# Kernel tuning notes

Measured on AMD Instinct MI355X. Metric: run time of the kernel, lower is better.

## Reference

```python
import jax, jax.numpy as jnp
import numpy as np

N = 50000
E = 800000
F_IN = 256
C = 64  # embedding_size, heads=1
EDGE_DIM = 2
NEG_SLOPE = 0.01


def setup_inputs() -> dict:
    key = jax.random.key(0)
    ks = jax.random.split(key, 12)
    s = 1.0 / np.sqrt(C)
    return {
        "x": jax.random.normal(ks[0], (N, F_IN), jnp.float32),
        "edge_index": jax.random.randint(ks[1], (2, E), 0, N, jnp.int64),
        "edge_attr": jax.random.normal(ks[2], (E, EDGE_DIM), jnp.float32),
        "Wf": jax.random.normal(ks[3], (F_IN, C), jnp.float32) / np.sqrt(F_IN),
        "bf": jnp.zeros((C,), jnp.float32),
        "Wq": jax.random.normal(ks[4], (C, C), jnp.float32) * s,
        "bq": jnp.zeros((C,), jnp.float32),
        "Wk": jax.random.normal(ks[5], (C, C), jnp.float32) * s,
        "bk": jnp.zeros((C,), jnp.float32),
        "Wv": jax.random.normal(ks[6], (C, C), jnp.float32) * s,
        "bv": jnp.zeros((C,), jnp.float32),
        "We": jax.random.normal(ks[7], (EDGE_DIM, C), jnp.float32) / np.sqrt(EDGE_DIM),
        "Wskip": jax.random.normal(ks[8], (C, C), jnp.float32) * s,
        "bskip": jnp.zeros((C,), jnp.float32),
    }


def reference(x, edge_index, edge_attr, Wf, bf, Wq, bq, Wk, bk, Wv, bv, We, Wskip, bskip):
    n = x.shape[0]
    src, dst = edge_index[0], edge_index[1]
    inv_sqrt_c = 1.0 / np.sqrt(C)

    h = jax.nn.leaky_relu(x @ Wf + bf, NEG_SLOPE)
    e = edge_attr @ We  # [E, C] edge embedding (lin_edge, no bias), same each layer

    for _ in range(3):
        q = h @ Wq + bq
        k = h @ Wk + bk
        v = h @ Wv + bv
        kj = k[src] + e                                  # [E, C] key + edge feat
        alpha = jnp.sum(q[dst] * kj, axis=-1) * inv_sqrt_c  # [E]
        # per-destination softmax
        m = jax.ops.segment_max(alpha, dst, num_segments=n)
        ex = jnp.exp(alpha - m[dst])
        den = jax.ops.segment_sum(ex, dst, num_segments=n)
        a = ex / den[dst]                                # [E]
        msg = (v[src] + e) * a[:, None]                  # [E, C]
        agg = jax.ops.segment_sum(msg, dst, num_segments=n)  # [N, C]
        h = jax.nn.leaky_relu(agg + h @ Wskip + bskip, NEG_SLOPE)  # root_weight skip
    return h
```

## Files before the change

kernel.cpp:

```cpp
#include <hip/hip_runtime.h>
#include <hip/hip_fp16.h>

#define NN 50000
#define NE 800000
#define FIN 256
#define C 64
#define NEG_SLOPE 0.01f
#define SCAN_BLOCKS ((NN + 255) / 256)
#define NBUCK 196
#define BCAP 8192
#define EB_CHUNK 2048
#define EB_BLOCKS ((NE + EB_CHUNK - 1) / EB_CHUNK)

typedef float f32x16 __attribute__((ext_vector_type(16)));

__device__ __forceinline__ float leaky(float v) { return v > 0.f ? v : NEG_SLOPE * v; }

__global__ __launch_bounds__(256) void k_tw(const float* __restrict__ Wq,
                                            const float* __restrict__ Wk,
                                            const float* __restrict__ Wv,
                                            const float* __restrict__ Ws,
                                            float* __restrict__ Wt) {
    const int idx = blockIdx.x * 256 + threadIdx.x;
    if (idx >= 4 * 64 * 64) return;
    const int m = idx >> 12, r = idx & 4095, c = r >> 6, k = r & 63;
    const float* W = (m == 0) ? Wq : (m == 1) ? Wk : (m == 2) ? Wv : Ws;
    Wt[idx] = W[k * 64 + c];
}

__global__ __launch_bounds__(256) void k_feat(const float* __restrict__ x,
                                              const float* __restrict__ Wf,
                                              const float* __restrict__ bf,
                                              float* __restrict__ h) {
    __shared__ float4 Sx[64][33];
    const int t = threadIdx.x;
    const int lane = t & 63;
    const int q = __builtin_amdgcn_readfirstlane(t) >> 6;
    const int base = blockIdx.x * 64;

    const float4* x4 = (const float4*)x;
    float4 acc[4];
#pragma unroll
    for (int cp = 0; cp < 4; ++cp) acc[cp] = make_float4(0.f, 0.f, 0.f, 0.f);

#define FRAG(wreg, xs)                                                      \
    acc[0].x = fmaf(xs, wreg[0],  acc[0].x);                                \
    acc[0].y = fmaf(xs, wreg[1],  acc[0].y);                                \
    acc[0].z = fmaf(xs, wreg[2],  acc[0].z);                                \
    acc[0].w = fmaf(xs, wreg[3],  acc[0].w);                                \
    acc[1].x = fmaf(xs, wreg[4],  acc[1].x);                                \
    acc[1].y = fmaf(xs, wreg[5],  acc[1].y);                                \
    acc[1].z = fmaf(xs, wreg[6],  acc[1].z);                                \
    acc[1].w = fmaf(xs, wreg[7],  acc[1].w);                                \
    acc[2].x = fmaf(xs, wreg[8],  acc[2].x);                                \
    acc[2].y = fmaf(xs, wreg[9],  acc[2].y);                                \
    acc[2].z = fmaf(xs, wreg[10], acc[2].z);                                \
    acc[2].w = fmaf(xs, wreg[11], acc[2].w);                                \
    acc[3].x = fmaf(xs, wreg[12], acc[3].x);                                \
    acc[3].y = fmaf(xs, wreg[13], acc[3].y);                                \
    acc[3].z = fmaf(xs, wreg[14], acc[3].z);                                \
    acc[3].w = fmaf(xs, wreg[15], acc[3].w);

    for (int ph = 0; ph < 2; ++ph) {
#pragma unroll
        for (int i = 0; i < 8; ++i) {
            const int idx = t + i * 256;
            const int row = idx >> 5, c = idx & 31;
            int nn = base + row; if (nn >= NN) nn = NN - 1;
            Sx[row][c] = x4[(size_t)nn * 64 + ph * 32 + c];
        }
        __syncthreads();

        const float* wbase = Wf + (size_t)(ph * 128) * 64 + q * 16;
#pragma unroll
        for (int j = 0; j < 32; ++j) {
            const float4 xv = Sx[lane][j];
            const float* wrow = wbase + (size_t)j * 256;
            f32x16 w0_, w1_, w2_, w3_;
            asm volatile("s_load_dwordx16 %0, %4, 0x0\n\t"
                         "s_load_dwordx16 %1, %4, 0x100\n\t"
                         "s_load_dwordx16 %2, %4, 0x200\n\t"
                         "s_load_dwordx16 %3, %4, 0x300\n\t"
                         "s_waitcnt lgkmcnt(0)"
                         : "=&s"(w0_), "=&s"(w1_), "=&s"(w2_), "=&s"(w3_)
                         : "s"(wrow));
            FRAG(w0_, xv.x)
            FRAG(w1_, xv.y)
            FRAG(w2_, xv.z)
            FRAG(w3_, xv.w)
        }
        __syncthreads();
    }
#undef FRAG

    float4* O = (float4*)Sx;
    const float4* bf4 = (const float4*)bf;
#pragma unroll
    for (int cp = 0; cp < 4; ++cp) {
        const float4 b = bf4[q * 4 + cp];
        float4 r;
        r.x = leaky(acc[cp].x + b.x); r.y = leaky(acc[cp].y + b.y);
        r.z = leaky(acc[cp].z + b.z); r.w = leaky(acc[cp].w + b.w);
        O[lane * 17 + q * 4 + cp] = r;
    }
    __syncthreads();
#pragma unroll
    for (int i = 0; i < 4; ++i) {
        const int idx = t + i * 256;
        const int row = idx >> 4, c = idx & 15;
        const int nn = base + row;
        if (nn < NN) ((float4*)h)[(size_t)nn * 16 + c] = O[row * 17 + c];
    }
}

#define QKVS_NPB 32

__global__ __launch_bounds__(256) void k_qkvs(const float* __restrict__ h,
                                              const float* __restrict__ Wt,
                                              const float* __restrict__ bq,
                                              const float* __restrict__ bk,
                                              const float* __restrict__ bv,
                                              const float* __restrict__ bs,
                                              float* __restrict__ qkvs) {
    __shared__ float4 Sh[QKVS_NPB][16];
    const int t = threadIdx.x;
    const int lane = t & 63;
    const int wid = __builtin_amdgcn_readfirstlane(t) >> 6;
    const int base = blockIdx.x * QKVS_NPB;

    const float4* h4 = (const float4*)h;
#pragma unroll
    for (int i = 0; i < 2; ++i) {
        const int idx = t + i * 256;
        const int row = idx >> 4, c = idx & 15;
        int n = base + row; if (n >= NN) n = NN - 1;
        Sh[row][c] = h4[(size_t)n * 16 + c];
    }

    const bool kv = (wid < 2);
    const int wn = (wid & 1) << 4;

    const int mA = kv ? 1 : 0;
    const int mB = kv ? 2 : 3;
    const float4* wa4 = (const float4*)(Wt + ((size_t)mA << 12) + ((size_t)lane << 6));
    const float4* wb4 = (const float4*)(Wt + ((size_t)mB << 12) + ((size_t)lane << 6));
    float4 wa[16], wb[16];
#pragma unroll
    for (int j = 0; j < 16; ++j) { wa[j] = wa4[j]; wb[j] = wb4[j]; }
    const float biasA = kv ? bk[lane] : bq[lane];
    const float biasB = kv ? bv[lane] : bs[lane];

    __syncthreads();

#pragma unroll 2
    for (int i = 0; i < 16; ++i) {
        const int n = base + wn + i;
        float a0 = 0.f, a1 = 0.f, a2 = 0.f, a3 = 0.f;
        float b0 = 0.f, b1 = 0.f, b2 = 0.f, b3 = 0.f;
#pragma unroll
        for (int j = 0; j < 16; ++j) {
            const float4 xv = Sh[wn + i][j];
            a0 = fmaf(xv.x, wa[j].x, a0); a1 = fmaf(xv.y, wa[j].y, a1);
            a2 = fmaf(xv.z, wa[j].z, a2); a3 = fmaf(xv.w, wa[j].w, a3);
            b0 = fmaf(xv.x, wb[j].x, b0); b1 = fmaf(xv.y, wb[j].y, b1);
            b2 = fmaf(xv.z, wb[j].z, b2); b3 = fmaf(xv.w, wb[j].w, b3);
        }
        const float A = ((a0 + a1) + (a2 + a3)) + biasA;
        const float B = ((b0 + b1) + (b2 + b3)) + biasB;
        if (n < NN) {
            float* orow = qkvs + (size_t)n * 192;
            if (kv) {
                ((__half2*)(orow + 64))[lane] = __floats2half2_rn(A, B);
            } else {
                orow[lane] = A;
                orow[128 + lane] = B;
            }
        }
    }
}

__global__ __launch_bounds__(256) void k_bucket(const int* __restrict__ ei,
                                                const float* __restrict__ eattr,
                                                int* __restrict__ gcur,
                                                uint2* __restrict__ ebuck) {
    __shared__ int hist[NBUCK], lbase[NBUCK], lcur[NBUCK];
    const int t = threadIdx.x;
    const int base = blockIdx.x * EB_CHUNK;
    if (t < NBUCK) { hist[t] = 0; lcur[t] = 0; }
    __syncthreads();

    int dcache[8];
#pragma unroll
    for (int i = 0; i < 8; ++i) {
        const int e = base + i * 256 + t;
        int d = -1;
        if (e < NE) {
            d = ei[NE + e];
            atomicAdd(&hist[d >> 8], 1);
        }
        dcache[i] = d;
    }
    __syncthreads();
    if (t < NBUCK && hist[t] > 0)
        lbase[t] = atomicAdd(&gcur[t], hist[t]);
    __syncthreads();

#pragma unroll
    for (int i = 0; i < 8; ++i) {
        const int e = base + i * 256 + t;
        const int d = dcache[i];
        if (d >= 0) {
            const int b = d >> 8;
            const int rank = atomicAdd(&lcur[b], 1);
            const __half2 a = __floats2half2_rn(eattr[e * 2], eattr[e * 2 + 1]);
            const unsigned src = (unsigned)ei[e];
            ebuck[(size_t)b * BCAP + lbase[b] + rank] =
                make_uint2(((unsigned)d << 16) | src, *(const unsigned*)&a);
        }
    }
}

__global__ __launch_bounds__(256) void k_fin_deg(const int* __restrict__ gcur,
                                                 const uint2* __restrict__ ebuck,
                                                 int* __restrict__ deg) {
    __shared__ int dcnt[256];
    const int t = threadIdx.x;
    const int b = blockIdx.x;
    dcnt[t] = 0;
    __syncthreads();
    const int n = gcur[b];
    for (int i = t; i < n; i += 256) {
        const unsigned x = ebuck[(size_t)b * BCAP + i].x;
        atomicAdd(&dcnt[(x >> 16) & 255], 1);
    }
    __syncthreads();
    const int idx = b * 256 + t;
    if (idx < NN) deg[idx] = dcnt[t];
}

__global__ __launch_bounds__(256) void k_blocksum(const int* __restrict__ deg,
                                                  int* __restrict__ bsum) {
    __shared__ int sh[256];
    const int t = threadIdx.x;
    const int idx = blockIdx.x * 256 + t;
    sh[t] = (idx < NN) ? deg[idx] : 0;
    __syncthreads();
#pragma unroll
    for (int off = 128; off > 0; off >>= 1) {
        if (t < off) sh[t] += sh[t + off];
        __syncthreads();
    }
    if (t == 0) bsum[blockIdx.x] = sh[0];
}

__global__ __launch_bounds__(256) void k_scanb(const int* __restrict__ bsum,
                                               int* __restrict__ boff) {
    __shared__ int sh[256];
    const int t = threadIdx.x;
    const int v = (t < SCAN_BLOCKS) ? bsum[t] : 0;
    sh[t] = v;
    __syncthreads();
#pragma unroll
    for (int off = 1; off < 256; off <<= 1) {
        const int x = (t >= off) ? sh[t - off] : 0;
        __syncthreads();
        sh[t] += x;
        __syncthreads();
    }
    if (t < SCAN_BLOCKS) boff[t] = sh[t] - v;
}

__global__ __launch_bounds__(256) void k_writeptr(const int* __restrict__ deg,
                                                  const int* __restrict__ boff,
                                                  int* __restrict__ row_ptr) {
    __shared__ int sh[256];
    const int t = threadIdx.x;
    const int idx = blockIdx.x * 256 + t;
    const int v = (idx < NN) ? deg[idx] : 0;
    sh[t] = v;
    __syncthreads();
#pragma unroll
    for (int off = 1; off < 256; off <<= 1) {
        const int x = (t >= off) ? sh[t - off] : 0;
        __syncthreads();
        sh[t] += x;
        __syncthreads();
    }
    if (idx < NN) row_ptr[idx] = boff[blockIdx.x] + sh[t] - v;
    if (idx == 0) row_ptr[NN] = NE;
}

__global__ __launch_bounds__(256) void k_fin_scat(const int* __restrict__ gcur,
                                                  const uint2* __restrict__ ebuck,
                                                  const int* __restrict__ row_ptr,
                                                  uint2* __restrict__ erec) {
    __shared__ int pcur[256];
    const int t = threadIdx.x;
    const int b = blockIdx.x;
    const int idx = b * 256 + t;
    pcur[t] = (idx < NN) ? row_ptr[idx] : 0;
    __syncthreads();
    const int n = gcur[b];
    for (int i = t; i < n; i += 256) {
        const uint2 rec = ebuck[(size_t)b * BCAP + i];
        const int d = (rec.x >> 16) & 255;
        const int pos = atomicAdd(&pcur[d], 1);
        erec[pos] = make_uint2(rec.x & 0xFFFFu, rec.y);
    }
}

__global__ __launch_bounds__(256) void k_conv(const int* __restrict__ row_ptr,
                                              const uint2* __restrict__ erec,
                                              const float* __restrict__ We,
                                              const float* __restrict__ qkvs,
                                              float* __restrict__ hout) {
    const int t = threadIdx.x;
    const int lane = t & 63;
    const int g = lane >> 4;
    const int p = lane & 15;
    const int wv = __builtin_amdgcn_readfirstlane(t) >> 6;
    const int d = blockIdx.x * 4 + wv;
    if (d >= NN) return;

    const float* qrow = qkvs + (size_t)d * 192;
    const float4 q4  = *(const float4*)(qrow + 4 * p);
    const float4 w0  = *(const float4*)(We + 4 * p);
    const float4 w1  = *(const float4*)(We + 64 + 4 * p);

    float pg0 = q4.x * w0.x + q4.y * w0.y + q4.z * w0.z + q4.w * w0.w;
    float pg1 = q4.x * w1.x + q4.y * w1.y + q4.z * w1.z + q4.w * w1.w;
#pragma unroll
    for (int mask = 1; mask <= 8; mask <<= 1) {
        pg0 += __shfl_xor(pg0, mask);
        pg1 += __shfl_xor(pg1, mask);
    }
    const float g0 = pg0, g1 = pg1;

    const int i0 = row_ptr[d], i1 = row_ptr[d + 1];
    const char* kvbase = (const char*)qkvs + 256 + ((size_t)p << 4);

    float m = -1e30f, l = 0.f, S1 = 0.f, S2 = 0.f;
    float4 acc = make_float4(0.f, 0.f, 0.f, 0.f);

    int i = i0 + g;
    for (; i + 4 < i1; i += 8) {
        const uint2 ra = erec[i];
        const uint2 rb = erec[i + 4];
        const __half2 aha = *(const __half2*)&ra.y;
        const __half2 ahb = *(const __half2*)&rb.y;
        const float a0a = __low2float(aha), a1a = __high2float(aha);
        const float a0b = __low2float(ahb), a1b = __high2float(ahb);
        const float4 kva = *(const float4*)(kvbase + (size_t)ra.x * 768);
        const float4 kvb = *(const float4*)(kvbase + (size_t)rb.x * 768);
        const __half2* ha = (const __half2*)&kva;
        const __half2* hb = (const __half2*)&kvb;
        const float ka0 = __low2float(ha[0]), va0 = __high2float(ha[0]);
        const float ka1 = __low2float(ha[1]), va1 = __high2float(ha[1]);
        const float ka2 = __low2float(ha[2]), va2 = __high2float(ha[2]);
        const float ka3 = __low2float(ha[3]), va3 = __high2float(ha[3]);
        const float kb0 = __low2float(hb[0]), vb0 = __high2float(hb[0]);
        const float kb1 = __low2float(hb[1]), vb1 = __high2float(hb[1]);
        const float kb2 = __low2float(hb[2]), vb2 = __high2float(hb[2]);
        const float kb3 = __low2float(hb[3]), vb3 = __high2float(hb[3]);
        float da = q4.x * ka0 + q4.y * ka1 + q4.z * ka2 + q4.w * ka3;
        float db = q4.x * kb0 + q4.y * kb1 + q4.z * kb2 + q4.w * kb3;
        da += __shfl_xor(da, 1);  db += __shfl_xor(db, 1);
        da += __shfl_xor(da, 2);  db += __shfl_xor(db, 2);
        da += __shfl_xor(da, 4);  db += __shfl_xor(db, 4);
        da += __shfl_xor(da, 8);  db += __shfl_xor(db, 8);
        const float Pa = (da + g0 * a0a + g1 * a1a) * 0.125f;
        const float Pb = (db + g0 * a0b + g1 * a1b) * 0.125f;
        const float mn = fmaxf(m, fmaxf(Pa, Pb));
        const float s  = __expf(m - mn);
        const float ea = __expf(Pa - mn);
        const float eb = __expf(Pb - mn);
        l = l * s + ea + eb;
        acc.x = acc.x * s + va0 * ea + vb0 * eb;
        acc.y = acc.y * s + va1 * ea + vb1 * eb;
        acc.z = acc.z * s + va2 * ea + vb2 * eb;
        acc.w = acc.w * s + va3 * ea + vb3 * eb;
        S1 = S1 * s + a0a * ea + a0b * eb;
        S2 = S2 * s + a1a * ea + a1b * eb;
        m = mn;
    }
    for (; i < i1; i += 4) {
        const uint2 r = erec[i];
        const __half2 ah = *(const __half2*)&r.y;
        const float a0 = __low2float(ah), a1 = __high2float(ah);
        const float4 kvl = *(const float4*)(kvbase + (size_t)r.x * 768);
        const __half2* hv = (const __half2*)&kvl;
        const float kf0 = __low2float(hv[0]), vf0 = __high2float(hv[0]);
        const float kf1 = __low2float(hv[1]), vf1 = __high2float(hv[1]);
        const float kf2 = __low2float(hv[2]), vf2 = __high2float(hv[2]);
        const float kf3 = __low2float(hv[3]), vf3 = __high2float(hv[3]);
        float dot = q4.x * kf0 + q4.y * kf1 + q4.z * kf2 + q4.w * kf3;
        dot += __shfl_xor(dot, 1);
        dot += __shfl_xor(dot, 2);
        dot += __shfl_xor(dot, 4);
        dot += __shfl_xor(dot, 8);
        const float P = (dot + g0 * a0 + g1 * a1) * 0.125f;
        const float mn = fmaxf(m, P);
        const float s = __expf(m - mn);
        const float e = __expf(P - mn);
        l = l * s + e;
        acc.x = acc.x * s + vf0 * e;
        acc.y = acc.y * s + vf1 * e;
        acc.z = acc.z * s + vf2 * e;
        acc.w = acc.w * s + vf3 * e;
        S1 = S1 * s + a0 * e;
        S2 = S2 * s + a1 * e;
        m = mn;
    }

#pragma unroll
    for (int mask = 16; mask <= 32; mask <<= 1) {
        const float mo  = __shfl_xor(m, mask);
        const float lo  = __shfl_xor(l, mask);
        const float axo = __shfl_xor(acc.x, mask);
        const float ayo = __shfl_xor(acc.y, mask);
        const float azo = __shfl_xor(acc.z, mask);
        const float awo = __shfl_xor(acc.w, mask);
        const float S1o = __shfl_xor(S1, mask);
        const float S2o = __shfl_xor(S2, mask);
        const float mn = fmaxf(m, mo);
        const float sA = __expf(m - mn);
        const float sB = __expf(mo - mn);
        l     = l * sA + lo * sB;
        acc.x = acc.x * sA + axo * sB;
        acc.y = acc.y * sA + ayo * sB;
        acc.z = acc.z * sA + azo * sB;
        acc.w = acc.w * sA + awo * sB;
        S1    = S1 * sA + S1o * sB;
        S2    = S2 * sA + S2o * sB;
        m = mn;
    }

    if (lane < 16) {
        const float inv = (l > 0.f) ? 1.f / l : 0.f;
        const float4 sk = *(const float4*)(qrow + 128 + 4 * p);
        float4 r;
        r.x = leaky((acc.x + S1 * w0.x + S2 * w1.x) * inv + sk.x);
        r.y = leaky((acc.y + S1 * w0.y + S2 * w1.y) * inv + sk.y);
        r.z = leaky((acc.z + S1 * w0.z + S2 * w1.z) * inv + sk.z);
        r.w = leaky((acc.w + S1 * w0.w + S2 * w1.w) * inv + sk.w);
        *(float4*)(hout + (size_t)d * C + 4 * p) = r;
    }
}

extern "C" void kernel_launch(void* const* d_in, const int* in_sizes, int n_in,
                              void* d_out, int out_size, void* d_ws, size_t ws_size,
                              hipStream_t stream) {
    const float* x     = (const float*)d_in[0];
    const int*   ei    = (const int*)d_in[1];
    const float* eattr = (const float*)d_in[2];
    const float* Wf    = (const float*)d_in[3];
    const float* bf    = (const float*)d_in[4];
    const float* Wq    = (const float*)d_in[5];
    const float* bq    = (const float*)d_in[6];
    const float* Wk    = (const float*)d_in[7];
    const float* bk    = (const float*)d_in[8];
    const float* Wv    = (const float*)d_in[9];
    const float* bv    = (const float*)d_in[10];
    const float* We    = (const float*)d_in[11];
    const float* Ws    = (const float*)d_in[12];
    const float* bs    = (const float*)d_in[13];
    float* out = (float*)d_out;

    char* p = (char*)d_ws;
    float*  h       = (float*)p;  p += (size_t)NN * C * 4;
    float*  qkvs    = (float*)p;  p += (size_t)NN * 192 * 4;
    float*  Wt      = (float*)p;  p += (size_t)4 * 64 * 64 * 4;
    int*    deg     = (int*)p;    p += (size_t)NN * 4;
    int*    row_ptr = (int*)p;    p += (size_t)(NN + 1) * 4;
    int*    bsum    = (int*)p;    p += (size_t)SCAN_BLOCKS * 4;
    int*    boff    = (int*)p;    p += (size_t)SCAN_BLOCKS * 4;
    int*    gcur    = (int*)p;    p += (size_t)NBUCK * 4;
    uint2*  erec    = (uint2*)p;  p += (size_t)NE * 8;
    uint2*  ebuck   = (uint2*)p;  p += (size_t)NBUCK * BCAP * 8;

    k_tw<<<64, 256, 0, stream>>>(Wq, Wk, Wv, Ws, Wt);
    hipMemsetAsync(gcur, 0, (size_t)NBUCK * 4, stream);
    k_bucket<<<EB_BLOCKS, 256, 0, stream>>>(ei, eattr, gcur, ebuck);
    k_fin_deg<<<NBUCK, 256, 0, stream>>>(gcur, ebuck, deg);
    k_blocksum<<<SCAN_BLOCKS, 256, 0, stream>>>(deg, bsum);
    k_scanb<<<1, 256, 0, stream>>>(bsum, boff);
    k_writeptr<<<SCAN_BLOCKS, 256, 0, stream>>>(deg, boff, row_ptr);
    k_fin_scat<<<NBUCK, 256, 0, stream>>>(gcur, ebuck, row_ptr, erec);

    const int feat_grid = (NN + 63) / 64;
    const int qkvs_grid = (NN + QKVS_NPB - 1) / QKVS_NPB;

    k_feat<<<feat_grid, 256, 0, stream>>>(x, Wf, bf, h);

    for (int layer = 0; layer < 3; ++layer) {
        k_qkvs<<<qkvs_grid, 256, 0, stream>>>(h, Wt, bq, bk, bv, bs, qkvs);
        float* hout = (layer == 2) ? out : h;
        k_conv<<<(NN + 3) / 4, 256, 0, stream>>>(row_ptr, erec, We, qkvs, hout);
    }
}
```

Baseline: 463.1 us.

## Restructure QKVS GEMM to node-per-lane with scalar-loaded weight tiles

Rewrites the per-layer Q/K/V/skip projection so each lane owns one node and each wave computes a 16-column slice for 64 nodes. Weights are read directly from the original row-major matrices into scalar registers with s_load_dwordx16 and broadcast to all lanes, replacing per-lane vector weight registers and cross-lane dot-product reductions. The weight transpose kernel and its workspace are dropped. The cost is a full lgkmcnt wait on every scalar load batch, strided LDS reads of h per lane, and strided per-lane global stores.

```diff
diff --git a/kernel.cpp b/kernel.cpp
--- a/kernel.cpp
+++ b/kernel.cpp
@@ -15,18 +15,6 @@
 typedef float f32x16 __attribute__((ext_vector_type(16)));
 
 __device__ __forceinline__ float leaky(float v) { return v > 0.f ? v : NEG_SLOPE * v; }
-
-__global__ __launch_bounds__(256) void k_tw(const float* __restrict__ Wq,
-                                            const float* __restrict__ Wk,
-                                            const float* __restrict__ Wv,
-                                            const float* __restrict__ Ws,
-                                            float* __restrict__ Wt) {
-    const int idx = blockIdx.x * 256 + threadIdx.x;
-    if (idx >= 4 * 64 * 64) return;
-    const int m = idx >> 12, r = idx & 4095, c = r >> 6, k = r & 63;
-    const float* W = (m == 0) ? Wq : (m == 1) ? Wk : (m == 2) ? Wv : Ws;
-    Wt[idx] = W[k * 64 + c];
-}
 
 __global__ __launch_bounds__(256) void k_feat(const float* __restrict__ x,
                                               const float* __restrict__ Wf,
@@ -113,70 +101,99 @@
     }
 }
 
-#define QKVS_NPB 32
-
 __global__ __launch_bounds__(256) void k_qkvs(const float* __restrict__ h,
-                                              const float* __restrict__ Wt,
+                                              const float* __restrict__ Wq,
+                                              const float* __restrict__ Wk,
+                                              const float* __restrict__ Wv,
+                                              const float* __restrict__ Ws,
                                               const float* __restrict__ bq,
                                               const float* __restrict__ bk,
                                               const float* __restrict__ bv,
                                               const float* __restrict__ bs,
                                               float* __restrict__ qkvs) {
-    __shared__ float4 Sh[QKVS_NPB][16];
+    __shared__ float4 Sh[64][17];
     const int t = threadIdx.x;
     const int lane = t & 63;
-    const int wid = __builtin_amdgcn_readfirstlane(t) >> 6;
-    const int base = blockIdx.x * QKVS_NPB;
+    const int w = __builtin_amdgcn_readfirstlane(t) >> 6;
+    const int base = blockIdx.x * 64;
 
     const float4* h4 = (const float4*)h;
 #pragma unroll
-    for (int i = 0; i < 2; ++i) {
+    for (int i = 0; i < 4; ++i) {
         const int idx = t + i * 256;
         const int row = idx >> 4, c = idx & 15;
         int n = base + row; if (n >= NN) n = NN - 1;
         Sh[row][c] = h4[(size_t)n * 16 + c];
     }
-
-    const bool kv = (wid < 2);
-    const int wn = (wid & 1) << 4;
-
-    const int mA = kv ? 1 : 0;
-    const int mB = kv ? 2 : 3;
-    const float4* wa4 = (const float4*)(Wt + ((size_t)mA << 12) + ((size_t)lane << 6));
-    const float4* wb4 = (const float4*)(Wt + ((size_t)mB << 12) + ((size_t)lane << 6));
-    float4 wa[16], wb[16];
-#pragma unroll
-    for (int j = 0; j < 16; ++j) { wa[j] = wa4[j]; wb[j] = wb4[j]; }
-    const float biasA = kv ? bk[lane] : bq[lane];
-    const float biasB = kv ? bv[lane] : bs[lane];
-
-    __syncthreads();
-
-#pragma unroll 2
-    for (int i = 0; i < 16; ++i) {
-        const int n = base + wn + i;
-        float a0 = 0.f, a1 = 0.f, a2 = 0.f, a3 = 0.f;
-        float b0 = 0.f, b1 = 0.f, b2 = 0.f, b3 = 0.f;
-#pragma unroll
-        for (int j = 0; j < 16; ++j) {
-            const float4 xv = Sh[wn + i][j];
-            a0 = fmaf(xv.x, wa[j].x, a0); a1 = fmaf(xv.y, wa[j].y, a1);
-            a2 = fmaf(xv.z, wa[j].z, a2); a3 = fmaf(xv.w, wa[j].w, a3);
-            b0 = fmaf(xv.x, wb[j].x, b0); b1 = fmaf(xv.y, wb[j].y, b1);
-            b2 = fmaf(xv.z, wb[j].z, b2); b3 = fmaf(xv.w, wb[j].w, b3);
-        }
-        const float A = ((a0 + a1) + (a2 + a3)) + biasA;
-        const float B = ((b0 + b1) + (b2 + b3)) + biasB;
-        if (n < NN) {
-            float* orow = qkvs + (size_t)n * 192;
-            if (kv) {
-                ((__half2*)(orow + 64))[lane] = __floats2half2_rn(A, B);
-            } else {
-                orow[lane] = A;
-                orow[128 + lane] = B;
-            }
-        }
-    }
+    __syncthreads();
+
+    const int n = base + lane;
+    const bool ok = (n < NN);
+    float* orow = qkvs + (size_t)n * 192;
+    const int c0 = w << 4;
+
+#define MATMUL(Wp, A)                                                        \
+    _Pragma("unroll")                                                        \
+    for (int j = 0; j < 16; ++j) {                                           \
+        const float4 xv = Sh[lane][j];                                       \
+        const float* wrow = (Wp) + (size_t)(4 * j) * 64 + c0;                \
+        f32x16 w0_, w1_, w2_, w3_;                                           \
+        asm volatile("s_load_dwordx16 %0, %4, 0x0\n\t"                       \
+                     "s_load_dwordx16 %1, %4, 0x100\n\t"                     \
+                     "s_load_dwordx16 %2, %4, 0x200\n\t"                     \
+                     "s_load_dwordx16 %3, %4, 0x300\n\t"                     \
+                     "s_waitcnt lgkmcnt(0)"                                  \
+                     : "=&s"(w0_), "=&s"(w1_), "=&s"(w2_), "=&s"(w3_)        \
+                     : "s"(wrow));                                           \
+        _Pragma("unroll")                                                    \
+        for (int i = 0; i < 16; ++i) {                                       \
+            A[i] = fmaf(xv.x, w0_[i], A[i]);                                 \
+            A[i] = fmaf(xv.y, w1_[i], A[i]);                                 \
+            A[i] = fmaf(xv.z, w2_[i], A[i]);                                 \
+            A[i] = fmaf(xv.w, w3_[i], A[i]);                                 \
+        }                                                                    \
+    }
+
+    {
+        float a[16];
+#pragma unroll
+        for (int i = 0; i < 16; ++i) a[i] = bq[c0 + i];
+        MATMUL(Wq, a)
+        if (ok) {
+#pragma unroll
+            for (int i = 0; i < 4; ++i)
+                *(float4*)(orow + c0 + 4 * i) =
+                    make_float4(a[4 * i], a[4 * i + 1], a[4 * i + 2], a[4 * i + 3]);
+        }
+    }
+    {
+        float ak[16], av[16];
+#pragma unroll
+        for (int i = 0; i < 16; ++i) ak[i] = bk[c0 + i];
+        MATMUL(Wk, ak)
+#pragma unroll
+        for (int i = 0; i < 16; ++i) av[i] = bv[c0 + i];
+        MATMUL(Wv, av)
+        if (ok) {
+            __half2* kvh = (__half2*)(orow + 64);
+#pragma unroll
+            for (int i = 0; i < 16; ++i)
+                kvh[c0 + i] = __floats2half2_rn(ak[i], av[i]);
+        }
+    }
+    {
+        float a[16];
+#pragma unroll
+        for (int i = 0; i < 16; ++i) a[i] = bs[c0 + i];
+        MATMUL(Ws, a)
+        if (ok) {
+#pragma unroll
+            for (int i = 0; i < 4; ++i)
+                *(float4*)(orow + 128 + c0 + 4 * i) =
+                    make_float4(a[4 * i], a[4 * i + 1], a[4 * i + 2], a[4 * i + 3]);
+        }
+    }
+#undef MATMUL
 }
 
 __global__ __launch_bounds__(256) void k_bucket(const int* __restrict__ ei,
@@ -469,7 +486,6 @@
     char* p = (char*)d_ws;
     float*  h       = (float*)p;  p += (size_t)NN * C * 4;
     float*  qkvs    = (float*)p;  p += (size_t)NN * 192 * 4;
-    float*  Wt      = (float*)p;  p += (size_t)4 * 64 * 64 * 4;
     int*    deg     = (int*)p;    p += (size_t)NN * 4;
     int*    row_ptr = (int*)p;    p += (size_t)(NN + 1) * 4;
     int*    bsum    = (int*)p;    p += (size_t)SCAN_BLOCKS * 4;
@@ -478,7 +494,6 @@
     uint2*  erec    = (uint2*)p;  p += (size_t)NE * 8;
     uint2*  ebuck   = (uint2*)p;  p += (size_t)NBUCK * BCAP * 8;
 
-    k_tw<<<64, 256, 0, stream>>>(Wq, Wk, Wv, Ws, Wt);
     hipMemsetAsync(gcur, 0, (size_t)NBUCK * 4, stream);
     k_bucket<<<EB_BLOCKS, 256, 0, stream>>>(ei, eattr, gcur, ebuck);
     k_fin_deg<<<NBUCK, 256, 0, stream>>>(gcur, ebuck, deg);
@@ -487,13 +502,13 @@
     k_writeptr<<<SCAN_BLOCKS, 256, 0, stream>>>(deg, boff, row_ptr);
     k_fin_scat<<<NBUCK, 256, 0, stream>>>(gcur, ebuck, row_ptr, erec);
 
-    const int feat_grid = (NN + 63) / 64;
-    const int qkvs_grid = (NN + QKVS_NPB - 1) / QKVS_NPB;
-
-    k_feat<<<feat_grid, 256, 0, stream>>>(x, Wf, bf, h);
+    const int gemm_grid = (NN + 63) / 64;
+
+    k_feat<<<gemm_grid, 256, 0, stream>>>(x, Wf, bf, h);
 
     for (int layer = 0; layer < 3; ++layer) {
-        k_qkvs<<<qkvs_grid, 256, 0, stream>>>(h, Wt, bq, bk, bv, bs, qkvs);
+        k_qkvs<<<gemm_grid, 256, 0, stream>>>(h, Wq, Wk, Wv, Ws,
+                                              bq, bk, bv, bs, qkvs);
         float* hout = (layer == 2) ? out : h;
         k_conv<<<(NN + 3) / 4, 256, 0, stream>>>(row_ptr, erec, We, qkvs, hout);
     }
```

Measured after the change: 743.2 us. 1.6x slower.
